# Performance work log

Hardware: AMD Instinct MI355X
Metric: run time of the kernel (lower is better)

The kernel has to match this reference:

```python
import jax, jax.numpy as jnp
import numpy as np

B, T, D = 16, 2048, 512
DB, K, TOPK, WIN = 128, 7, 16, 64
GATE_CAP = 0.5
STRAND_CAP = 0.5
_PHI = 1.618033988749895
_PSI = -0.6180339887498949


def _ln(x, w, b):
    mu = jnp.mean(x, -1, keepdims=True)
    var = jnp.var(x, -1, keepdims=True)
    return (x - mu) * jax.lax.rsqrt(var + 1e-5) * w + b


def setup_inputs() -> dict:
    key = jax.random.key(0)
    ks = jax.random.split(key, 20)
    def nrm(i, shape, scale=1.0):
        return jax.random.normal(ks[i], shape, dtype=jnp.float32) * jnp.float32(scale)
    return {
        'X_write': nrm(0, (B, T, D)),
        'X_read': nrm(1, (B, T, D)),
        'slots': nrm(2, (B, K, DB)),
        'W0': nrm(3, (D, D), D ** -0.5),
        'ln_write_w': jnp.ones((D,), jnp.float32),
        'ln_write_b': jnp.zeros((D,), jnp.float32),
        'W_V': nrm(4, (D, DB), D ** -0.5),
        'W_K_slot': nrm(5, (DB, DB), DB ** -0.5),
        'slot_key_bias': nrm(6, (K, DB), 2.0),
        'W_gate_w': nrm(7, (2 * DB, DB), (2 * DB) ** -0.5),
        'W_gate_b': jnp.full((DB,), -2.0, jnp.float32),
        'ln_strand_w': jnp.ones((DB,), jnp.float32),
        'ln_strand_b': jnp.zeros((DB,), jnp.float32),
        'Ws_Q': nrm(8, (DB, DB), DB ** -0.5),
        'Ws_K': nrm(9, (DB, DB), DB ** -0.5),
        'Ws_V': nrm(10, (DB, DB), DB ** -0.5),
        'lambda_strand': nrm(11, (DB,), 0.5),
        'W_Q_read': nrm(12, (D, DB), D ** -0.5),
        'W_K_read': nrm(13, (DB, DB), DB ** -0.5),
        'W_V_read': nrm(14, (DB, D), DB ** -0.5),
        'render_coeffs': nrm(15, (K, 3, D), 0.2),
        'slot_temps': jnp.ones((K,), jnp.float32),
    }


def _forward(X_write, X_read, slots, W0, ln_write_w, ln_write_b, W_V, W_K_slot,
             slot_key_bias, W_gate_w, W_gate_b, ln_strand_w, ln_strand_b,
             Ws_Q, Ws_K, Ws_V, lambda_strand, W_Q_read, W_K_read, W_V_read,
             render_coeffs, slot_temps):
    scale = jnp.float32(DB ** -0.5)
    W0_sg = jax.lax.stop_gradient(W0)
    X_n = _ln(X_write, ln_write_w, ln_write_b)

    # ---- windowed salience + topk pair selection (no-grad in original) ----
    X_nsg = jax.lax.stop_gradient(X_n)
    X_W0 = X_nsg @ W0_sg.T                      # [B,T,D]
    NEG = jnp.float32(-1e30)
    sal = []
    for o in range(1, WIN + 1):                 # offset j = i - o, fixed small loop
        s = jnp.sum(X_nsg[:, o:, :] * X_W0[:, :-o, :], axis=-1)  # [B, T-o]
        sal.append(jnp.pad(s, ((0, 0), (o, 0)), constant_values=NEG))
    sal = jnp.stack(sal, axis=-1).reshape(B, T * WIN)
    _, flat_idx = jax.lax.top_k(sal, TOPK)      # [B, TOPK]
    i_idx = flat_idx // WIN
    j_idx = i_idx - (flat_idx % WIN + 1)

    # ---- gather pairs, salience-weighted relation vector ----
    x_newer = jnp.take_along_axis(X_n, i_idx[:, :, None], axis=1)   # [B,TOPK,D]
    x_older = jnp.take_along_axis(X_n, j_idx[:, :, None], axis=1)
    pair_sal = jnp.sum(x_newer * (x_older @ W0_sg.T), axis=-1)      # [B,TOPK]
    alpha = jax.nn.softmax(pair_sal, axis=-1)
    rel = (x_newer - x_older) @ W_V                                 # [B,TOPK,DB]
    R_t = jnp.einsum('bk,bkd->bd', alpha, rel)                      # [B,DB]

    # ---- gated slot write ----
    slot_keys = slots @ W_K_slot + slot_key_bias                    # [B,K,DB]
    compat = jnp.einsum('bkd,bd->bk', slot_keys, R_t) * scale * jax.nn.softplus(slot_temps)
    sw = jax.nn.softmax(compat, axis=-1)
    weighted_R = sw[:, :, None] * R_t[:, None, :]                   # [B,K,DB]
    g = jax.nn.sigmoid(jnp.concatenate([slots, weighted_R], -1) @ W_gate_w + W_gate_b)
    slots_upd = (1.0 - g) * slots + g * weighted_R

    # ---- K x K strand mixer ----
    Bn = _ln(slots_upd, ln_strand_w, ln_strand_b)
    sa = jax.nn.softmax(jnp.einsum('bqd,bkd->bqk', Bn @ Ws_Q, Bn @ Ws_K) * scale, axis=-1)
    ctx = sa @ (Bn @ Ws_V)
    slots_next = slots_upd + ctx * jnp.clip(jnp.tanh(lambda_strand), -STRAND_CAP, STRAND_CAP)

    # ---- aux losses ----
    L_persist = jnp.mean((slots_next - slots) ** 2)
    nrm = jnp.maximum(jnp.linalg.norm(slots_next, axis=-1, keepdims=True), 1e-12)
    Bnorm = slots_next / nrm
    cos = jnp.einsum('bkd,bjd->bkj', Bnorm, Bnorm)
    off = ~jnp.eye(K, dtype=bool)
    L_div = jnp.mean((cos ** 2)[:, off])

    # ---- directional gated read attention ----
    q_r = X_read @ W_Q_read                                         # [B,T,DB]
    k_r = slots_next @ W_K_read                                     # [B,K,DB]
    v_r = slots_next @ W_V_read                                     # [B,K,D]
    scores = jnp.einsum('btd,bkd->btk', q_r, k_r) * scale
    q_mean = jnp.mean(X_read, axis=1)                               # [B,D]
    w0q = q_mean @ W0_sg.T
    denom = jnp.float32(_PHI - _PSI)
    phi_q = (w0q - _PSI * q_mean) / denom
    psi_q = (_PHI * q_mean - w0q) / denom
    phi_mag = jnp.linalg.norm(phi_q, axis=-1, keepdims=True)
    psi_mag = jnp.linalg.norm(psi_q, axis=-1, keepdims=True)
    total = phi_mag + psi_mag + 1e-6
    basis = jnp.concatenate([jnp.ones_like(phi_mag), phi_mag / total, psi_mag / total], -1)  # [B,3]
    gate = jnp.clip(jnp.tanh(jnp.einsum('bi,kid->bkd', basis, render_coeffs)), -GATE_CAP, GATE_CAP)
    z = jnp.einsum('btk,bkd->btd', jax.nn.softmax(scores, axis=-1), v_r * gate)
    return z, slots_next, L_persist, L_div


def reference(X_write, X_read, slots, W0, ln_write_w, ln_write_b, W_V, W_K_slot,
              slot_key_bias, W_gate_w, W_gate_b, ln_strand_w, ln_strand_b,
              Ws_Q, Ws_K, Ws_V, lambda_strand, W_Q_read, W_K_read, W_V_read,
              render_coeffs, slot_temps):
    return _forward(X_write, X_read, slots, W0, ln_write_w, ln_write_b, W_V, W_K_slot,
                    slot_key_bias, W_gate_w, W_gate_b, ln_strand_w, ln_strand_b,
                    Ws_Q, Ws_K, Ws_V, lambda_strand, W_Q_read, W_K_read, W_V_read,
                    render_coeffs, slot_temps)
```

## Files before the change

kernel.cpp:

```cpp
#include <hip/hip_runtime.h>
#include <math.h>

#define B_ 16
#define T_ 2048
#define D_ 512
#define DB_ 128
#define K_ 7
#define TOPK_ 16
#define WIN_ 64

static constexpr float SCALE_ = 0.08838834764831845f;
static constexpr float PHI_ = 1.618033988749895f;
static constexpr float PSI_ = -0.6180339887498949f;
static constexpr float INV_DENOM_ = 0.4472135954999579f;
static constexpr float NEGV = -1e30f;
static constexpr float NEGINF = -3.402823466e38f;

typedef __attribute__((ext_vector_type(8))) __bf16 bf16x8;
typedef __attribute__((ext_vector_type(8))) unsigned short u16x8;
typedef __attribute__((ext_vector_type(4))) float f32x4;

__device__ inline float softplusf(float x){
    return fmaxf(x, 0.f) + log1pf(expf(-fabsf(x)));
}
__device__ inline unsigned short f2bf(float x){
    unsigned int u = __float_as_uint(x);
    unsigned int r = (u + 0x7FFFu + ((u >> 16) & 1u)) >> 16;
    return (unsigned short)r;
}
__device__ inline float bf2f(unsigned short h){
    return __uint_as_float(((unsigned int)h) << 16);
}
__device__ inline bf16x8 ld_bf8(const unsigned short* p){
    u16x8 r = *(const u16x8*)p;
    return __builtin_bit_cast(bf16x8, r);
}
__device__ inline unsigned int pkbf(float a, float b){
    unsigned int r;
    asm("v_cvt_pk_bf16_f32 %0, %1, %2" : "=v"(r) : "v"(a), "v"(b));
    return r;
}
typedef __attribute__((address_space(3))) unsigned int as3_u32;
typedef const __attribute__((address_space(1))) unsigned int as1_u32c;
__device__ inline void gload16(const void* g, void* l){
    __builtin_amdgcn_global_load_lds((as1_u32c*)g, (as3_u32*)l, 16, 0, 0);
}

__global__ __launch_bounds__(256) void prep_kernel(const float* __restrict__ X,
                                                   const float* __restrict__ w,
                                                   const float* __restrict__ b,
                                                   unsigned short* __restrict__ Xh,
                                                   unsigned short* __restrict__ Xl,
                                                   const float* __restrict__ W0,
                                                   unsigned short* __restrict__ Wh,
                                                   unsigned short* __restrict__ Wl,
                                                   const float* __restrict__ Xr,
                                                   float* __restrict__ qpart)
{
    int bx = blockIdx.x;
    int tid = threadIdx.x;
    if (bx < 4096) {
        int lane = tid & 63, wv = tid >> 6;
        int row = bx * 8 + wv * 2;
        float4 wv0 = *(const float4*)(w + lane*4);
        float4 wv1 = *(const float4*)(w + 256 + lane*4);
        float4 bv0 = *(const float4*)(b + lane*4);
        float4 bv1 = *(const float4*)(b + 256 + lane*4);
        #pragma unroll
        for (int rr = 0; rr < 2; rr++) {
            const float* x = X + (size_t)(row + rr) * D_;
            float4 v0 = *(const float4*)(x + lane*4);
            float4 v1 = *(const float4*)(x + 256 + lane*4);
            float s  = v0.x+v0.y+v0.z+v0.w + v1.x+v1.y+v1.z+v1.w;
            float ss = v0.x*v0.x+v0.y*v0.y+v0.z*v0.z+v0.w*v0.w
                     + v1.x*v1.x+v1.y*v1.y+v1.z*v1.z+v1.w*v1.w;
            #pragma unroll
            for (int off = 32; off; off >>= 1) { s += __shfl_xor(s, off); ss += __shfl_xor(ss, off); }
            float mu = s * (1.f/512.f);
            float rs = rsqrtf(ss*(1.f/512.f) - mu*mu + 1e-5f);
            float o0 = (v0.x - mu)*rs*wv0.x + bv0.x;
            float o1 = (v0.y - mu)*rs*wv0.y + bv0.y;
            float o2 = (v0.z - mu)*rs*wv0.z + bv0.z;
            float o3 = (v0.w - mu)*rs*wv0.w + bv0.w;
            float o4 = (v1.x - mu)*rs*wv1.x + bv1.x;
            float o5 = (v1.y - mu)*rs*wv1.y + bv1.y;
            float o6 = (v1.z - mu)*rs*wv1.z + bv1.z;
            float o7 = (v1.w - mu)*rs*wv1.w + bv1.w;
            unsigned short h0 = f2bf(o0), h1 = f2bf(o1), h2 = f2bf(o2), h3 = f2bf(o3);
            unsigned short h4 = f2bf(o4), h5 = f2bf(o5), h6 = f2bf(o6), h7 = f2bf(o7);
            uint2 hA; hA.x = (unsigned int)h0 | ((unsigned int)h1 << 16);
                      hA.y = (unsigned int)h2 | ((unsigned int)h3 << 16);
            uint2 hB; hB.x = (unsigned int)h4 | ((unsigned int)h5 << 16);
                      hB.y = (unsigned int)h6 | ((unsigned int)h7 << 16);
            uint2 lA; lA.x = (unsigned int)f2bf(o0 - bf2f(h0)) | ((unsigned int)f2bf(o1 - bf2f(h1)) << 16);
                      lA.y = (unsigned int)f2bf(o2 - bf2f(h2)) | ((unsigned int)f2bf(o3 - bf2f(h3)) << 16);
            uint2 lB; lB.x = (unsigned int)f2bf(o4 - bf2f(h4)) | ((unsigned int)f2bf(o5 - bf2f(h5)) << 16);
                      lB.y = (unsigned int)f2bf(o6 - bf2f(h6)) | ((unsigned int)f2bf(o7 - bf2f(h7)) << 16);
            unsigned short* xh = Xh + (size_t)(row + rr) * D_;
            unsigned short* xl = Xl + (size_t)(row + rr) * D_;
            *(uint2*)(xh + lane*4) = hA;
            *(uint2*)(xh + 256 + lane*4) = hB;
            *(uint2*)(xl + lane*4) = lA;
            *(uint2*)(xl + 256 + lane*4) = lB;
        }
    } else if (bx < 4352) {
        int gid = (bx - 4096) * 256 + tid;
        float4 v = ((const float4*)W0)[gid];
        unsigned short h0 = f2bf(v.x), h1 = f2bf(v.y), h2 = f2bf(v.z), h3 = f2bf(v.w);
        ushort4 hv = make_ushort4(h0, h1, h2, h3);
        ushort4 lv = make_ushort4(f2bf(v.x - bf2f(h0)), f2bf(v.y - bf2f(h1)),
                                  f2bf(v.z - bf2f(h2)), f2bf(v.w - bf2f(h3)));
        *(ushort4*)&Wh[(size_t)gid*4] = hv;
        *(ushort4*)&Wl[(size_t)gid*4] = lv;
    } else {
        int idx = bx - 4352;
        int b_ = idx >> 5, c = idx & 31;
        const float* base = Xr + ((size_t)(b_*T_ + c*64)) * D_;
        float s0 = 0.f, s1 = 0.f;
        for (int t = 0; t < 64; t++) {
            s0 += base[(size_t)t*D_ + tid];
            s1 += base[(size_t)t*D_ + tid + 256];
        }
        qpart[((size_t)b_*32 + c)*D_ + tid] = s0;
        qpart[((size_t)b_*32 + c)*D_ + tid + 256] = s1;
    }
}

__global__ __launch_bounds__(256) void gemm_xw0_mfma(const unsigned short* __restrict__ Ah,
                                                     const unsigned short* __restrict__ Al,
                                                     const unsigned short* __restrict__ Wh,
                                                     const unsigned short* __restrict__ Wl,
                                                     float* __restrict__ Cf)
{
    __shared__ __align__(16) unsigned short sAh[128*32], sAl[128*32], sBh[128*32], sBl[128*32];
    int t0 = blockIdx.x * 128, d0 = blockIdx.y * 128;
    int tid = threadIdx.x;
    int lane = tid & 63, wid = tid >> 6;
    int wr = wid >> 1, wc = wid & 1;
    int fr = lane & 15;
    int kc2 = ((((lane >> 4) + (fr >> 1)) & 3) * 8);

    f32x4 acc[4][4];
    #pragma unroll
    for (int m = 0; m < 4; m++)
        #pragma unroll
        for (int n = 0; n < 4; n++) acc[m][n] = (f32x4){0.f,0.f,0.f,0.f};

    const unsigned short* gs = (wid==0) ? Ah : (wid==1) ? Al : (wid==2) ? Wh : Wl;
    unsigned short* ls = (wid==0) ? sAh : (wid==1) ? sAl : (wid==2) ? sBh : sBl;
    int rowoff = (wid < 2) ? t0 : d0;
    int cch = ((lane & 3) - ((lane >> 3) & 3)) & 3;
    const unsigned short* gbase = gs + (size_t)(rowoff + (lane >> 2))*512 + cch*8;

    for (int kk = 0; kk < 512; kk += 32) {
        #pragma unroll
        for (int i = 0; i < 8; i++)
            gload16(gbase + (size_t)(16*i)*512 + kk, ls + i*512);
        __syncthreads();

        bf16x8 ahf[4], alf[4], bhf[4], blf[4];
        #pragma unroll
        for (int m = 0; m < 4; m++) {
            int r = (wr*64 + m*16 + fr)*32 + kc2;
            ahf[m] = ld_bf8(&sAh[r]);
            alf[m] = ld_bf8(&sAl[r]);
        }
        #pragma unroll
        for (int n = 0; n < 4; n++) {
            int r = (wc*64 + n*16 + fr)*32 + kc2;
            bhf[n] = ld_bf8(&sBh[r]);
            blf[n] = ld_bf8(&sBl[r]);
        }
        #pragma unroll
        for (int m = 0; m < 4; m++)
            #pragma unroll
            for (int n = 0; n < 4; n++) {
                acc[m][n] = __builtin_amdgcn_mfma_f32_16x16x32_bf16(bhf[n], ahf[m], acc[m][n], 0, 0, 0);
                acc[m][n] = __builtin_amdgcn_mfma_f32_16x16x32_bf16(bhf[n], alf[m], acc[m][n], 0, 0, 0);
                acc[m][n] = __builtin_amdgcn_mfma_f32_16x16x32_bf16(blf[n], ahf[m], acc[m][n], 0, 0, 0);
            }
        __syncthreads();
    }

    #pragma unroll
    for (int m = 0; m < 4; m++) {
        int t = t0 + wr*64 + m*16 + fr;
        #pragma unroll
        for (int n = 0; n < 4; n++) {
            int dbase = d0 + wc*64 + n*16 + (lane >> 4)*4;
            *(f32x4*)&Cf[(size_t)t*512 + dbase] = acc[m][n];
        }
    }
}

__global__ __launch_bounds__(256) void sal_mfma(const unsigned short* __restrict__ Xh,
                                                const unsigned short* __restrict__ Xl,
                                                const float* __restrict__ Cf,
                                                float* __restrict__ sal)
{
    int b = blockIdx.x, i0 = blockIdx.y * 64;
    __shared__ __align__(16) unsigned short sAh[64*32], sAl[64*32], sBh[128*32], sBl[128*32];
    int tid = threadIdx.x;
    int lane = tid & 63, wcw = tid >> 6;
    int fr = lane & 15;
    int kc2 = ((((lane >> 4) + (fr >> 1)) & 3) * 8);

    const unsigned short* XhB = Xh + (size_t)b*T_*D_;
    const unsigned short* XlB = Xl + (size_t)b*T_*D_;
    const float* CfB = Cf + (size_t)b*T_*D_;

    f32x4 acc[4][2];
    #pragma unroll
    for (int m = 0; m < 4; m++) { acc[m][0] = (f32x4){0.f,0.f,0.f,0.f}; acc[m][1] = (f32x4){0.f,0.f,0.f,0.f}; }

    int ar = tid >> 2, ac = tid & 3;
    int aslot = (ac + (ar >> 1)) & 3;
    int brow = tid >> 1, bhh = tid & 1;
    int jrow = i0 - 64 + brow;

    for (int kk = 0; kk < 512; kk += 32) {
        *(uint4*)&sAh[ar*32 + aslot*8] = *(const uint4*)(XhB + (size_t)(i0 + ar)*512 + kk + ac*8);
        *(uint4*)&sAl[ar*32 + aslot*8] = *(const uint4*)(XlB + (size_t)(i0 + ar)*512 + kk + ac*8);
        #pragma unroll
        for (int cc = 0; cc < 2; cc++) {
            int c = 2*bhh + cc;
            int slot = (c + (brow >> 1)) & 3;
            uint4 hv, lv;
            if (jrow >= 0) {
                const float* src = CfB + (size_t)jrow*512 + kk + c*8;
                float4 v0 = *(const float4*)src;
                float4 v1 = *(const float4*)(src + 4);
                unsigned int h01 = pkbf(v0.x, v0.y), h23 = pkbf(v0.z, v0.w);
                unsigned int h45 = pkbf(v1.x, v1.y), h67 = pkbf(v1.z, v1.w);
                float r0 = v0.x - __uint_as_float(h01 << 16);
                float r1 = v0.y - __uint_as_float(h01 & 0xFFFF0000u);
                float r2 = v0.z - __uint_as_float(h23 << 16);
                float r3 = v0.w - __uint_as_float(h23 & 0xFFFF0000u);
                float r4 = v1.x - __uint_as_float(h45 << 16);
                float r5 = v1.y - __uint_as_float(h45 & 0xFFFF0000u);
                float r6 = v1.z - __uint_as_float(h67 << 16);
                float r7 = v1.w - __uint_as_float(h67 & 0xFFFF0000u);
                hv.x = h01; hv.y = h23; hv.z = h45; hv.w = h67;
                lv.x = pkbf(r0, r1); lv.y = pkbf(r2, r3); lv.z = pkbf(r4, r5); lv.w = pkbf(r6, r7);
            } else {
                hv = make_uint4(0,0,0,0); lv = make_uint4(0,0,0,0);
            }
            *(uint4*)&sBh[brow*32 + slot*8] = hv;
            *(uint4*)&sBl[brow*32 + slot*8] = lv;
        }
        __syncthreads();

        bf16x8 ahf[4], alf[4], bhf[2], blf[2];
        #pragma unroll
        for (int m = 0; m < 4; m++) {
            int r = (m*16 + fr)*32 + kc2;
            ahf[m] = ld_bf8(&sAh[r]);
            alf[m] = ld_bf8(&sAl[r]);
        }
        #pragma unroll
        for (int n = 0; n < 2; n++) {
            int r = (wcw*32 + n*16 + fr)*32 + kc2;
            bhf[n] = ld_bf8(&sBh[r]);
            blf[n] = ld_bf8(&sBl[r]);
        }
        #pragma unroll
        for (int m = 0; m < 4; m++)
            #pragma unroll
            for (int n = 0; n < 2; n++) {
                acc[m][n] = __builtin_amdgcn_mfma_f32_16x16x32_bf16(ahf[m], bhf[n], acc[m][n], 0, 0, 0);
                acc[m][n] = __builtin_amdgcn_mfma_f32_16x16x32_bf16(ahf[m], blf[n], acc[m][n], 0, 0, 0);
                acc[m][n] = __builtin_amdgcn_mfma_f32_16x16x32_bf16(alf[m], bhf[n], acc[m][n], 0, 0, 0);
            }
        __syncthreads();
    }

    float* salB = sal + (size_t)b*T_*WIN_;
    #pragma unroll
    for (int m = 0; m < 4; m++) {
        #pragma unroll
        for (int n = 0; n < 2; n++) {
            int jl = wcw*32 + n*16 + fr;
            #pragma unroll
            for (int r = 0; r < 4; r++) {
                int il = m*16 + (lane >> 4)*4 + r;
                int o = il - jl + 64;
                if (o >= 1 && o <= 64) {
                    int jg = i0 - 64 + jl;
                    salB[(size_t)(i0 + il)*WIN_ + (o - 1)] = (jg >= 0) ? acc[m][n][r] : NEGV;
                }
            }
        }
    }
}

__global__ __launch_bounds__(256) void topk_stage1(const float* __restrict__ sal,
                                                   float* __restrict__ cv, int* __restrict__ ci)
{
    int b = blockIdx.x, c = blockIdx.y;
    const float* s = sal + (size_t)b*(T_*WIN_) + (size_t)c*2048;
    int base = c*2048;
    int tid = threadIdx.x;
    int lane = tid & 63, wvi = tid >> 6;
    float lv[8]; int li[8];
    #pragma unroll
    for (int k = 0; k < 8; k++) { lv[k] = NEGINF; li[k] = 0x7FFFFFFF; }
    #pragma unroll
    for (int r = 0; r < 8; r++) {
        int p = tid + r*256;
        float v = s[p];
        int idx = base + p;
        if (v > lv[7]) {
            int k = 7;
            while (k > 0 && lv[k-1] < v) { lv[k] = lv[k-1]; li[k] = li[k-1]; k--; }
            lv[k] = v; li[k] = idx;
        }
    }
    float* cvo = cv + (((size_t)b*64 + c)*64) + wvi*16;
    int*   cio = ci + (((size_t)b*64 + c)*64) + wvi*16;
    int head = 0;
    for (int r = 0; r < 16; r++) {
        float bv = (head < 8) ? lv[head] : NEGINF;
        int   bi = (head < 8) ? li[head] : 0x7FFFFFFF;
        float wv_ = bv; int wi = bi;
        #pragma unroll
        for (int off = 1; off < 64; off <<= 1) {
            float v2 = __shfl_xor(wv_, off);
            int   i2 = __shfl_xor(wi, off);
            if (v2 > wv_ || (v2 == wv_ && i2 < wi)) { wv_ = v2; wi = i2; }
        }
        if (bv == wv_ && bi == wi) head++;
        if (lane == 0) { cvo[r] = wv_; cio[r] = wi; }
    }
}

__global__ __launch_bounds__(1024) void slot_kernel(
    const unsigned short* __restrict__ Xh, const unsigned short* __restrict__ Xl,
    const float* __restrict__ slots_in,
    const float* __restrict__ cv, const int* __restrict__ ci,
    const float* __restrict__ W_V, const float* __restrict__ W_K_slot, const float* __restrict__ skb,
    const float* __restrict__ Wg, const float* __restrict__ Wgb,
    const float* __restrict__ lnw, const float* __restrict__ lnb,
    const float* __restrict__ WsQ, const float* __restrict__ WsK, const float* __restrict__ WsV,
    const float* __restrict__ lambda_, const float* __restrict__ temps,
    float* __restrict__ snws, float* __restrict__ out_slots,
    float* __restrict__ lpP, float* __restrict__ lpD)
{
    int b = blockIdx.x, tid = threadIdx.x;
    int lane = tid & 63, wvi = tid >> 6;
    __shared__ float alpha[16];
    __shared__ int   tis[16], tjs[16];
    __shared__ float tvv[16]; __shared__ int tii[16];
    __shared__ float scv[256]; __shared__ int sci[256];
    __shared__ float y[D_];
    __shared__ float part[8][DB_];
    __shared__ float pf[1024];
    __shared__ float Rt[DB_];
    __shared__ float sl[K_][DB_];
    __shared__ float upd[K_][DB_];
    __shared__ float Bn[K_][DB_];
    __shared__ float qq[K_][DB_], kk2[K_][DB_], vv[K_][DB_];
    __shared__ float snsh[K_][DB_];
    __shared__ float swv[K_], compat[K_], mu7[K_], rs7[K_], nr7[K_], ldv[K_];
    __shared__ float sa[K_][K_];

    for (int p = tid; p < K_*DB_; p += 1024) sl[p>>7][p&127] = slots_in[(size_t)b*K_*DB_ + p];

    {
        const float* cvb = cv + (size_t)b*4096;
        const int*   cib = ci + (size_t)b*4096;
        float lv[4]; int li[4];
        #pragma unroll
        for (int k = 0; k < 4; k++) { lv[k] = NEGINF; li[k] = 0x7FFFFFFF; }
        #pragma unroll
        for (int r = 0; r < 4; r++) {
            int p = tid + r*1024;
            float v = cvb[p];
            int idx = cib[p];
            if (v > lv[3] || (v == lv[3] && idx < li[3])) {
                int k = 3;
                while (k > 0 && (lv[k-1] < v || (lv[k-1] == v && li[k-1] > idx))) {
                    lv[k] = lv[k-1]; li[k] = li[k-1]; k--;
                }
                lv[k] = v; li[k] = idx;
            }
        }
        int head = 0;
        for (int r = 0; r < 16; r++) {
            float bv = (head < 4) ? lv[head] : NEGINF;
            int   bi = (head < 4) ? li[head] : 0x7FFFFFFF;
            float wv_ = bv; int wi = bi;
            #pragma unroll
            for (int off = 1; off < 64; off <<= 1) {
                float v2 = __shfl_xor(wv_, off);
                int   i2 = __shfl_xor(wi, off);
                if (v2 > wv_ || (v2 == wv_ && i2 < wi)) { wv_ = v2; wi = i2; }
            }
            if (bv == wv_ && bi == wi) head++;
            if (lane == 0) { scv[wvi*16 + r] = wv_; sci[wvi*16 + r] = wi; }
        }
        __syncthreads();
        if (wvi == 0) {
            float mv[4]; int mi[4];
            #pragma unroll
            for (int k = 0; k < 4; k++) { mv[k] = NEGINF; mi[k] = 0x7FFFFFFF; }
            #pragma unroll
            for (int r = 0; r < 4; r++) {
                int p = lane + r*64;
                float v = scv[p]; int idx = sci[p];
                if (v > mv[3] || (v == mv[3] && idx < mi[3])) {
                    int k = 3;
                    while (k > 0 && (mv[k-1] < v || (mv[k-1] == v && mi[k-1] > idx))) {
                        mv[k] = mv[k-1]; mi[k] = mi[k-1]; k--;
                    }
                    mv[k] = v; mi[k] = idx;
                }
            }
            int head2 = 0;
            for (int r = 0; r < 16; r++) {
                float bv = (head2 < 4) ? mv[head2] : NEGINF;
                int   bi = (head2 < 4) ? mi[head2] : 0x7FFFFFFF;
                float wv_ = bv; int wi = bi;
                #pragma unroll
                for (int off = 1; off < 64; off <<= 1) {
                    float v2 = __shfl_xor(wv_, off);
                    int   i2 = __shfl_xor(wi, off);
                    if (v2 > wv_ || (v2 == wv_ && i2 < wi)) { wv_ = v2; wi = i2; }
                }
                if (bv == wv_ && bi == wi) head2++;
                if (lane == 0) { tvv[r] = wv_; tii[r] = wi; }
            }
        }
        __syncthreads();
    }
    if (tid < 16) {
        float v = tvv[tid];
        int flat = tii[tid];
        tis[tid] = flat >> 6;
        tjs[tid] = (flat >> 6) - ((flat & 63) + 1);
        float m = v;
        #pragma unroll
        for (int off = 8; off; off >>= 1) m = fmaxf(m, __shfl_xor(m, off, 16));
        float e = expf(v - m);
        float s = e;
        #pragma unroll
        for (int off = 8; off; off >>= 1) s += __shfl_xor(s, off, 16);
        alpha[tid] = e / s;
    }
    __syncthreads();

    if (tid < D_) {
        float acc = 0.f;
        #pragma unroll
        for (int k = 0; k < 16; k++) {
            int i = tis[k], j = tjs[k];
            float xi = bf2f(Xh[((size_t)b*T_ + i)*D_ + tid]) + bf2f(Xl[((size_t)b*T_ + i)*D_ + tid]);
            float xj = bf2f(Xh[((size_t)b*T_ + j)*D_ + tid]) + bf2f(Xl[((size_t)b*T_ + j)*D_ + tid]);
            acc += alpha[k] * (xi - xj);
        }
        y[tid] = acc;
    }
    __syncthreads();

    {
        int g = tid >> 7, d = tid & 127;
        float acc = 0.f;
        int e0 = g * 64;
        for (int e = e0; e < e0 + 64; e++) acc += y[e] * W_V[(size_t)e*DB_ + d];
        part[g][d] = acc;
    }
    __syncthreads();
    if (tid < DB_) {
        float acc = 0.f;
        #pragma unroll
        for (int g = 0; g < 8; g++) acc += part[g][tid];
        Rt[tid] = acc;
    }
    __syncthreads();

    if (tid < K_*DB_) {
        int k = tid >> 7, d = tid & 127;
        float acc = skb[k*DB_ + d];
        for (int e = 0; e < DB_; e++) acc += sl[k][e] * W_K_slot[(size_t)e*DB_ + d];
        qq[k][d] = acc * Rt[d];
    }
    __syncthreads();
    if (wvi < K_) {
        float acc = qq[wvi][lane] + qq[wvi][lane + 64];
        #pragma unroll
        for (int off = 32; off; off >>= 1) acc += __shfl_xor(acc, off);
        if (lane == 0) compat[wvi] = acc * SCALE_ * softplusf(temps[wvi]);
    }
    __syncthreads();
    if (tid == 0) {
        float m = compat[0];
        for (int k = 1; k < K_; k++) m = fmaxf(m, compat[k]);
        float ssum = 0.f;
        for (int k = 0; k < K_; k++) { float e = expf(compat[k]-m); swv[k] = e; ssum += e; }
        for (int k = 0; k < K_; k++) swv[k] /= ssum;
    }
    __syncthreads();

    if (tid < K_*DB_) {
        int k = tid >> 7, d = tid & 127;
        float swk = swv[k];
        float acc = Wgb[d];
        for (int e = 0; e < DB_; e++) acc += sl[k][e] * Wg[(size_t)e*DB_ + d];
        for (int e = 0; e < DB_; e++) acc += swk * Rt[e] * Wg[(size_t)(DB_+e)*DB_ + d];
        float g = 1.f / (1.f + expf(-acc));
        upd[k][d] = (1.f - g) * sl[k][d] + g * (swk * Rt[d]);
    }
    __syncthreads();

    if (wvi < K_) {
        float v0 = upd[wvi][lane], v1 = upd[wvi][lane + 64];
        float s = v0 + v1, ss = v0*v0 + v1*v1;
        #pragma unroll
        for (int off = 32; off; off >>= 1) { s += __shfl_xor(s, off); ss += __shfl_xor(ss, off); }
        if (lane == 0) {
            float mu = s / (float)DB_;
            mu7[wvi] = mu;
            rs7[wvi] = rsqrtf(ss/(float)DB_ - mu*mu + 1e-5f);
        }
    }
    __syncthreads();
    if (tid < K_*DB_) {
        int k = tid >> 7, d = tid & 127;
        Bn[k][d] = (upd[k][d] - mu7[k]) * rs7[k] * lnw[d] + lnb[d];
    }
    __syncthreads();

    if (tid < K_*DB_) {
        int k = tid >> 7, d = tid & 127;
        float aq = 0.f, ak = 0.f, av = 0.f;
        for (int e = 0; e < DB_; e++) {
            float bn = Bn[k][e];
            aq += bn * WsQ[(size_t)e*DB_ + d];
            ak += bn * WsK[(size_t)e*DB_ + d];
            av += bn * WsV[(size_t)e*DB_ + d];
        }
        qq[k][d] = aq; kk2[k][d] = ak; vv[k][d] = av;
    }
    __syncthreads();

    if (wvi < K_) {
        int j = lane >> 3, s = lane & 7;
        float acc = 0.f;
        if (j < K_) {
            int e0 = s * 16;
            for (int e = e0; e < e0 + 16; e++) acc += qq[wvi][e] * kk2[j][e];
        }
        #pragma unroll
        for (int off = 4; off; off >>= 1) acc += __shfl_xor(acc, off, 8);
        if (s == 0 && j < K_) sa[wvi][j] = acc * SCALE_;
    }
    __syncthreads();
    if (tid < K_) {
        float m = sa[tid][0];
        for (int j = 1; j < K_; j++) m = fmaxf(m, sa[tid][j]);
        float ssum = 0.f;
        for (int j = 0; j < K_; j++) { float e = expf(sa[tid][j]-m); sa[tid][j] = e; ssum += e; }
        for (int j = 0; j < K_; j++) sa[tid][j] /= ssum;
    }
    __syncthreads();

    if (tid < K_*DB_) {
        int k = tid >> 7, d = tid & 127;
        float lam = tanhf(lambda_[d]);
        lam = fminf(fmaxf(lam, -0.5f), 0.5f);
        float c = 0.f;
        #pragma unroll
        for (int j = 0; j < K_; j++) c += sa[k][j] * vv[j][d];
        float sn = upd[k][d] + c * lam;
        snsh[k][d] = sn;
        snws[((size_t)b*K_ + k)*DB_ + d] = sn;
        out_slots[((size_t)b*K_ + k)*DB_ + d] = sn;
    }
    __syncthreads();

    {
        float dsq = 0.f;
        if (tid < K_*DB_) {
            int k = tid >> 7, d = tid & 127;
            float dd = snsh[k][d] - sl[k][d];
            dsq = dd*dd;
        }
        pf[tid] = dsq;
        if (wvi < K_) {
            float v0 = snsh[wvi][lane], v1 = snsh[wvi][lane + 64];
            float ss = v0*v0 + v1*v1;
            #pragma unroll
            for (int off = 32; off; off >>= 1) ss += __shfl_xor(ss, off);
            if (lane == 0) nr7[wvi] = fmaxf(sqrtf(ss), 1e-12f);
        }
        __syncthreads();
        if (wvi == 0) {
            float s = 0.f;
            #pragma unroll
            for (int q = 0; q < 16; q++) s += pf[lane + q*64];
            #pragma unroll
            for (int off = 32; off; off >>= 1) s += __shfl_xor(s, off);
            if (lane == 0) lpP[b] = s;
        }
        if (wvi >= 1 && wvi <= K_) {
            int q = wvi - 1;
            float accq = 0.f;
            for (int j = 0; j < K_; j++) {
                if (j == q) continue;
                float dt = snsh[q][lane]*snsh[j][lane] + snsh[q][lane+64]*snsh[j][lane+64];
                #pragma unroll
                for (int off = 32; off; off >>= 1) dt += __shfl_xor(dt, off);
                float cs = dt / (nr7[q] * nr7[j]);
                accq += cs*cs;
            }
            if (lane == 0) ldv[q] = accq;
        }
        __syncthreads();
        if (tid == 0) {
            float s = 0.f;
            for (int q = 0; q < K_; q++) s += ldv[q];
            lpD[b] = s;
        }
    }
}

__global__ __launch_bounds__(256) void w0q_part_kernel(const float* __restrict__ qpart,
                                                       const float* __restrict__ W0,
                                                       float* __restrict__ w0p)
{
    int b = blockIdx.x, c = blockIdx.y, tid = threadIdx.x;
    __shared__ float qm[D_];
    for (int p = tid; p < D_; p += 256) {
        float s = 0.f;
        for (int cc = 0; cc < 32; cc++) s += qpart[((size_t)b*32 + cc)*D_ + p];
        qm[p] = s * (1.f/2048.f);
    }
    __syncthreads();
    int w = tid >> 6, lane = tid & 63;
    float ph = 0.f, ps = 0.f;
    for (int r = 0; r < 16; r++) {
        int d = c*64 + w*16 + r;
        const float* wr = W0 + (size_t)d*D_;
        float s = 0.f;
        #pragma unroll
        for (int q = 0; q < 8; q++) s += qm[lane + q*64] * wr[lane + q*64];
        #pragma unroll
        for (int off = 32; off; off >>= 1) s += __shfl_xor(s, off);
        float phi = (s - PSI_*qm[d]) * INV_DENOM_;
        float psi = (PHI_*qm[d] - s) * INV_DENOM_;
        ph += phi*phi; ps += psi*psi;
    }
    __shared__ float shp[4], shs[4];
    if (lane == 0) { shp[w] = ph; shs[w] = ps; }
    __syncthreads();
    if (tid == 0) {
        w0p[((size_t)b*8 + c)*2 + 0] = shp[0]+shp[1]+shp[2]+shp[3];
        w0p[((size_t)b*8 + c)*2 + 1] = shs[0]+shs[1]+shs[2]+shs[3];
    }
}

__global__ __launch_bounds__(256) void kqvg_kernel(
    const float* __restrict__ sn, const float* __restrict__ WKr,
    const float* __restrict__ WQr, const float* __restrict__ WVr,
    const float* __restrict__ rc, const float* __restrict__ w0p,
    const float* __restrict__ lpP, const float* __restrict__ lpD,
    float* __restrict__ kq, float* __restrict__ vg, float* __restrict__ loss_out)
{
    int b = blockIdx.x, k = blockIdx.y, tid = threadIdx.x;
    if (b == 0 && k == 0 && tid == 0) {
        float s = 0.f, s2 = 0.f;
        for (int bb = 0; bb < B_; bb++) { s += lpP[bb]; s2 += lpD[bb]; }
        loss_out[0] = s / (float)(B_*K_*DB_);
        loss_out[1] = s2 / (float)(B_*(K_*K_-K_));
    }
    float P = 0.f, Q = 0.f;
    #pragma unroll
    for (int c = 0; c < 8; c++) {
        P += w0p[((size_t)b*8 + c)*2 + 0];
        Q += w0p[((size_t)b*8 + c)*2 + 1];
    }
    float pm = sqrtf(P), qm2 = sqrtf(Q);
    float tot = pm + qm2 + 1e-6f;
    float b1 = pm / tot, b2 = qm2 / tot;

    __shared__ float sl[DB_], kr[DB_];
    if (tid < DB_) sl[tid] = sn[((size_t)b*K_ + k)*DB_ + tid];
    __syncthreads();
    if (tid < DB_) {
        float a = 0.f;
        for (int e = 0; e < DB_; e++) a += sl[e] * WKr[(size_t)e*DB_ + tid];
        kr[tid] = a;
    }
    __syncthreads();
    #pragma unroll
    for (int rep = 0; rep < 2; rep++) {
        int e = tid + rep*256;
        float a = 0.f;
        const float* wq = WQr + (size_t)e*DB_;
        for (int d = 0; d < DB_; d++) a += kr[d] * wq[d];
        kq[((size_t)b*K_ + k)*D_ + e] = a;
    }
    #pragma unroll
    for (int rep = 0; rep < 2; rep++) {
        int dd = tid + rep*256;
        float a = 0.f;
        for (int e = 0; e < DB_; e++) a += sl[e] * WVr[(size_t)e*D_ + dd];
        float gpre = rc[((size_t)k*3 + 0)*D_ + dd] + b1*rc[((size_t)k*3 + 1)*D_ + dd] + b2*rc[((size_t)k*3 + 2)*D_ + dd];
        float g = tanhf(gpre);
        g = fminf(fmaxf(g, -0.5f), 0.5f);
        vg[((size_t)b*K_ + k)*D_ + dd] = a * g;
    }
}

__global__ __launch_bounds__(256) void z_kernel(const float* __restrict__ Xr,
                                                const float* __restrict__ kq,
                                                const float* __restrict__ vg,
                                                float* __restrict__ z)
{
    int b = blockIdx.x;
    int t0 = blockIdx.y * 64;
    __shared__ float kqs[K_][D_];
    __shared__ float vgs[K_][D_];
    int tid = threadIdx.x;
    for (int p = tid; p < K_*D_; p += 256) {
        kqs[p>>9][p&511] = kq[(size_t)b*K_*D_ + p];
        vgs[p>>9][p&511] = vg[(size_t)b*K_*D_ + p];
    }
    __syncthreads();
    int lane = tid & 63, w = tid >> 6;
    for (int it = 0; it < 16; it++) {
        int t = t0 + w*16 + it;
        const float* x = Xr + ((size_t)b*T_ + t)*D_;
        float xr[8];
        float s[K_] = {0,0,0,0,0,0,0};
        #pragma unroll
        for (int r = 0; r < 8; r++) {
            int e = lane + r*64;
            xr[r] = x[e];
            #pragma unroll
            for (int k = 0; k < K_; k++) s[k] += xr[r] * kqs[k][e];
        }
        #pragma unroll
        for (int k = 0; k < K_; k++)
            for (int off = 32; off; off >>= 1) s[k] += __shfl_xor(s[k], off);
        float sc[K_];
        float m = NEGINF;
        #pragma unroll
        for (int k = 0; k < K_; k++) { sc[k] = s[k] * SCALE_; m = fmaxf(m, sc[k]); }
        float p[K_], ssum = 0.f;
        #pragma unroll
        for (int k = 0; k < K_; k++) { p[k] = expf(sc[k] - m); ssum += p[k]; }
        float inv = 1.f / ssum;
        float* zp = z + ((size_t)b*T_ + t)*D_;
        #pragma unroll
        for (int r = 0; r < 8; r++) {
            int e = lane + r*64;
            float a = 0.f;
            #pragma unroll
            for (int k = 0; k < K_; k++) a += p[k] * vgs[k][e];
            zp[e] = a * inv;
        }
    }
}

extern "C" void kernel_launch(void* const* d_in, const int* in_sizes, int n_in,
                              void* d_out, int out_size, void* d_ws, size_t ws_size,
                              hipStream_t stream)
{
    const float* X_write = (const float*)d_in[0];
    const float* X_read  = (const float*)d_in[1];
    const float* slots   = (const float*)d_in[2];
    const float* W0      = (const float*)d_in[3];
    const float* lnw_w   = (const float*)d_in[4];
    const float* lnw_b   = (const float*)d_in[5];
    const float* W_V     = (const float*)d_in[6];
    const float* W_K_slot= (const float*)d_in[7];
    const float* skb     = (const float*)d_in[8];
    const float* Wg      = (const float*)d_in[9];
    const float* Wgb     = (const float*)d_in[10];
    const float* lns_w   = (const float*)d_in[11];
    const float* lns_b   = (const float*)d_in[12];
    const float* WsQ     = (const float*)d_in[13];
    const float* WsK     = (const float*)d_in[14];
    const float* WsV     = (const float*)d_in[15];
    const float* lambda_ = (const float*)d_in[16];
    const float* WQr     = (const float*)d_in[17];
    const float* WKr     = (const float*)d_in[18];
    const float* WVr     = (const float*)d_in[19];
    const float* rc      = (const float*)d_in[20];
    const float* temps   = (const float*)d_in[21];

    const size_t NXD = (size_t)B_*T_*D_;
    unsigned short* Xh  = (unsigned short*)d_ws;
    unsigned short* Xl  = Xh + NXD;
    float* Cf           = (float*)(Xl + NXD);
    unsigned short* W0h = (unsigned short*)(Cf + NXD);
    unsigned short* W0l = W0h + (size_t)D_*D_;
    float* fscr  = (float*)(W0l + (size_t)D_*D_);
    float* qpart = fscr;
    float* w0p   = qpart + (size_t)B_*32*D_;
    float* snws  = w0p + 256;
    float* kq    = snws + (size_t)B_*K_*DB_;
    float* vg    = kq + (size_t)B_*K_*D_;
    float* cv    = vg + (size_t)B_*K_*D_;
    int*   ci    = (int*)(cv + (size_t)B_*64*64);
    float* lpP   = (float*)(ci + (size_t)B_*64*64);
    float* lpD   = lpP + 16;

    float* z_out     = (float*)d_out;
    float* slots_out = z_out + NXD;
    float* loss_out  = slots_out + (size_t)B_*K_*DB_;
    float* sal       = z_out;

    prep_kernel<<<dim3(4096 + 256 + 512), dim3(256), 0, stream>>>(
        X_write, lnw_w, lnw_b, Xh, Xl, W0, W0h, W0l, X_read, qpart);
    gemm_xw0_mfma<<<dim3(B_*T_/128, D_/128), dim3(256), 0, stream>>>(Xh, Xl, W0h, W0l, Cf);
    sal_mfma<<<dim3(B_, T_/64), dim3(256), 0, stream>>>(Xh, Xl, Cf, sal);
    topk_stage1<<<dim3(B_, 64), dim3(256), 0, stream>>>(sal, cv, ci);
    slot_kernel<<<dim3(B_), dim3(1024), 0, stream>>>(Xh, Xl, slots, cv, ci,
        W_V, W_K_slot, skb, Wg, Wgb, lns_w, lns_b, WsQ, WsK, WsV, lambda_, temps,
        snws, slots_out, lpP, lpD);
    w0q_part_kernel<<<dim3(B_, 8), dim3(256), 0, stream>>>(qpart, W0, w0p);
    kqvg_kernel<<<dim3(B_, K_), dim3(256), 0, stream>>>(snws, WKr, WQr, WVr, rc, w0p,
        lpP, lpD, kq, vg, loss_out);
    z_kernel<<<dim3(B_, T_/64), dim3(256), 0, stream>>>(X_read, kq, vg, z_out);
}
```

Measured before the change: 288.1 us.

## Double-buffer GEMM and salience loads, fold w0q into topk launch

The X·W0 GEMM now double-buffers its shared-memory tiles, so the next K-slice is fetched while the current one feeds MFMA, and one barrier per iteration is dropped. The salience kernel prefetches the next slice's global data into registers before running the current slice's MFMAs, and converts to bf16 hi/lo when writing to shared memory. The w0q_part work moves into extra blocks of topk_stage1, removing one kernel launch. The trade-off is doubled LDS use in the GEMM, which may lower occupancy, and higher register pressure in sal_mfma.

```diff
diff --git a/kernel.cpp b/kernel.cpp
--- a/kernel.cpp
+++ b/kernel.cpp
@@ -132,7 +132,7 @@
                                                      const unsigned short* __restrict__ Wl,
                                                      float* __restrict__ Cf)
 {
-    __shared__ __align__(16) unsigned short sAh[128*32], sAl[128*32], sBh[128*32], sBl[128*32];
+    __shared__ __align__(16) unsigned short sAh[2*128*32], sAl[2*128*32], sBh[2*128*32], sBl[2*128*32];
     int t0 = blockIdx.x * 128, d0 = blockIdx.y * 128;
     int tid = threadIdx.x;
     int lane = tid & 63, wid = tid >> 6;
@@ -147,27 +147,36 @@
         for (int n = 0; n < 4; n++) acc[m][n] = (f32x4){0.f,0.f,0.f,0.f};
 
     const unsigned short* gs = (wid==0) ? Ah : (wid==1) ? Al : (wid==2) ? Wh : Wl;
-    unsigned short* ls = (wid==0) ? sAh : (wid==1) ? sAl : (wid==2) ? sBh : sBl;
+    unsigned short* lsA = (wid==0) ? sAh : (wid==1) ? sAl : (wid==2) ? sBh : sBl;
     int rowoff = (wid < 2) ? t0 : d0;
     int cch = ((lane & 3) - ((lane >> 3) & 3)) & 3;
     const unsigned short* gbase = gs + (size_t)(rowoff + (lane >> 2))*512 + cch*8;
 
-    for (int kk = 0; kk < 512; kk += 32) {
-        #pragma unroll
-        for (int i = 0; i < 8; i++)
-            gload16(gbase + (size_t)(16*i)*512 + kk, ls + i*512);
+    #pragma unroll
+    for (int i = 0; i < 8; i++)
+        gload16(gbase + (size_t)(16*i)*512 + 0, lsA + i*512);
+
+    for (int t = 0; t < 16; t++) {
+        int cur = t & 1;
         __syncthreads();
-
+        if (t < 15) {
+            unsigned short* ls = lsA + (cur^1)*(128*32);
+            int kk = (t+1)*32;
+            #pragma unroll
+            for (int i = 0; i < 8; i++)
+                gload16(gbase + (size_t)(16*i)*512 + kk, ls + i*512);
+        }
+        int bo = cur*(128*32);
         bf16x8 ahf[4], alf[4], bhf[4], blf[4];
         #pragma unroll
         for (int m = 0; m < 4; m++) {
-            int r = (wr*64 + m*16 + fr)*32 + kc2;
+            int r = bo + (wr*64 + m*16 + fr)*32 + kc2;
             ahf[m] = ld_bf8(&sAh[r]);
             alf[m] = ld_bf8(&sAl[r]);
         }
         #pragma unroll
         for (int n = 0; n < 4; n++) {
-            int r = (wc*64 + n*16 + fr)*32 + kc2;
+            int r = bo + (wc*64 + n*16 + fr)*32 + kc2;
             bhf[n] = ld_bf8(&sBh[r]);
             blf[n] = ld_bf8(&sBl[r]);
         }
@@ -179,7 +188,6 @@
                 acc[m][n] = __builtin_amdgcn_mfma_f32_16x16x32_bf16(bhf[n], alf[m], acc[m][n], 0, 0, 0);
                 acc[m][n] = __builtin_amdgcn_mfma_f32_16x16x32_bf16(blf[n], ahf[m], acc[m][n], 0, 0, 0);
             }
-        __syncthreads();
     }
 
     #pragma unroll
@@ -218,38 +226,56 @@
     int brow = tid >> 1, bhh = tid & 1;
     int jrow = i0 - 64 + brow;
 
-    for (int kk = 0; kk < 512; kk += 32) {
-        *(uint4*)&sAh[ar*32 + aslot*8] = *(const uint4*)(XhB + (size_t)(i0 + ar)*512 + kk + ac*8);
-        *(uint4*)&sAl[ar*32 + aslot*8] = *(const uint4*)(XlB + (size_t)(i0 + ar)*512 + kk + ac*8);
+    uint4 rAh, rAl;
+    float4 rB0[2], rB1[2];
+
+    auto LOAD = [&](int kk){
+        rAh = *(const uint4*)(XhB + (size_t)(i0 + ar)*512 + kk + ac*8);
+        rAl = *(const uint4*)(XlB + (size_t)(i0 + ar)*512 + kk + ac*8);
+        #pragma unroll
+        for (int cc = 0; cc < 2; cc++) {
+            int c = 2*bhh + cc;
+            if (jrow >= 0) {
+                const float* src = CfB + (size_t)jrow*512 + kk + c*8;
+                rB0[cc] = *(const float4*)src;
+                rB1[cc] = *(const float4*)(src + 4);
+            } else {
+                rB0[cc] = make_float4(0.f,0.f,0.f,0.f);
+                rB1[cc] = make_float4(0.f,0.f,0.f,0.f);
+            }
+        }
+    };
+    auto WRITE = [&](){
+        *(uint4*)&sAh[ar*32 + aslot*8] = rAh;
+        *(uint4*)&sAl[ar*32 + aslot*8] = rAl;
         #pragma unroll
         for (int cc = 0; cc < 2; cc++) {
             int c = 2*bhh + cc;
             int slot = (c + (brow >> 1)) & 3;
             uint4 hv, lv;
-            if (jrow >= 0) {
-                const float* src = CfB + (size_t)jrow*512 + kk + c*8;
-                float4 v0 = *(const float4*)src;
-                float4 v1 = *(const float4*)(src + 4);
-                unsigned int h01 = pkbf(v0.x, v0.y), h23 = pkbf(v0.z, v0.w);
-                unsigned int h45 = pkbf(v1.x, v1.y), h67 = pkbf(v1.z, v1.w);
-                float r0 = v0.x - __uint_as_float(h01 << 16);
-                float r1 = v0.y - __uint_as_float(h01 & 0xFFFF0000u);
-                float r2 = v0.z - __uint_as_float(h23 << 16);
-                float r3 = v0.w - __uint_as_float(h23 & 0xFFFF0000u);
-                float r4 = v1.x - __uint_as_float(h45 << 16);
-                float r5 = v1.y - __uint_as_float(h45 & 0xFFFF0000u);
-                float r6 = v1.z - __uint_as_float(h67 << 16);
-                float r7 = v1.w - __uint_as_float(h67 & 0xFFFF0000u);
-                hv.x = h01; hv.y = h23; hv.z = h45; hv.w = h67;
-                lv.x = pkbf(r0, r1); lv.y = pkbf(r2, r3); lv.z = pkbf(r4, r5); lv.w = pkbf(r6, r7);
-            } else {
-                hv = make_uint4(0,0,0,0); lv = make_uint4(0,0,0,0);
-            }
+            float4 v0 = rB0[cc], v1 = rB1[cc];
+            unsigned int h01 = pkbf(v0.x, v0.y), h23 = pkbf(v0.z, v0.w);
+            unsigned int h45 = pkbf(v1.x, v1.y), h67 = pkbf(v1.z, v1.w);
+            float r0 = v0.x - __uint_as_float(h01 << 16);
+            float r1 = v0.y - __uint_as_float(h01 & 0xFFFF0000u);
+            float r2 = v0.z - __uint_as_float(h23 << 16);
+            float r3 = v0.w - __uint_as_float(h23 & 0xFFFF0000u);
+            float r4 = v1.x - __uint_as_float(h45 << 16);
+            float r5 = v1.y - __uint_as_float(h45 & 0xFFFF0000u);
+            float r6 = v1.z - __uint_as_float(h67 << 16);
+            float r7 = v1.w - __uint_as_float(h67 & 0xFFFF0000u);
+            hv.x = h01; hv.y = h23; hv.z = h45; hv.w = h67;
+            lv.x = pkbf(r0, r1); lv.y = pkbf(r2, r3); lv.z = pkbf(r4, r5); lv.w = pkbf(r6, r7);
             *(uint4*)&sBh[brow*32 + slot*8] = hv;
             *(uint4*)&sBl[brow*32 + slot*8] = lv;
         }
+    };
+
+    LOAD(0);
+    for (int t = 0; t < 16; t++) {
+        WRITE();
         __syncthreads();
-
+        int kkn = (t+1)*32;
         bf16x8 ahf[4], alf[4], bhf[2], blf[2];
         #pragma unroll
         for (int m = 0; m < 4; m++) {
@@ -263,6 +289,7 @@
             bhf[n] = ld_bf8(&sBh[r]);
             blf[n] = ld_bf8(&sBl[r]);
         }
+        if (t < 15) LOAD(kkn);
         #pragma unroll
         for (int m = 0; m < 4; m++)
             #pragma unroll
@@ -294,12 +321,47 @@
 }
 
 __global__ __launch_bounds__(256) void topk_stage1(const float* __restrict__ sal,
-                                                   float* __restrict__ cv, int* __restrict__ ci)
+                                                   float* __restrict__ cv, int* __restrict__ ci,
+                                                   const float* __restrict__ qpart,
+                                                   const float* __restrict__ W0,
+                                                   float* __restrict__ w0p)
 {
-    int b = blockIdx.x, c = blockIdx.y;
+    int b = blockIdx.x, tid = threadIdx.x;
+    if (blockIdx.y >= 64) {
+        int c = blockIdx.y - 64;
+        __shared__ float qm[D_];
+        for (int p = tid; p < D_; p += 256) {
+            float s = 0.f;
+            for (int cc = 0; cc < 32; cc++) s += qpart[((size_t)b*32 + cc)*D_ + p];
+            qm[p] = s * (1.f/2048.f);
+        }
+        __syncthreads();
+        int w = tid >> 6, lane = tid & 63;
+        float ph = 0.f, ps = 0.f;
+        for (int r = 0; r < 16; r++) {
+            int d = c*64 + w*16 + r;
+            const float* wr = W0 + (size_t)d*D_;
+            float s = 0.f;
+            #pragma unroll
+            for (int q = 0; q < 8; q++) s += qm[lane + q*64] * wr[lane + q*64];
+            #pragma unroll
+            for (int off = 32; off; off >>= 1) s += __shfl_xor(s, off);
+            float phi = (s - PSI_*qm[d]) * INV_DENOM_;
+            float psi = (PHI_*qm[d] - s) * INV_DENOM_;
+            ph += phi*phi; ps += psi*psi;
+        }
+        __shared__ float shp[4], shs[4];
+        if (lane == 0) { shp[w] = ph; shs[w] = ps; }
+        __syncthreads();
+        if (tid == 0) {
+            w0p[((size_t)b*8 + c)*2 + 0] = shp[0]+shp[1]+shp[2]+shp[3];
+            w0p[((size_t)b*8 + c)*2 + 1] = shs[0]+shs[1]+shs[2]+shs[3];
+        }
+        return;
+    }
+    int c = blockIdx.y;
     const float* s = sal + (size_t)b*(T_*WIN_) + (size_t)c*2048;
     int base = c*2048;
-    int tid = threadIdx.x;
     int lane = tid & 63, wvi = tid >> 6;
     float lv[8]; int li[8];
     #pragma unroll
@@ -623,41 +685,6 @@
     }
 }
 
-__global__ __launch_bounds__(256) void w0q_part_kernel(const float* __restrict__ qpart,
-                                                       const float* __restrict__ W0,
-                                                       float* __restrict__ w0p)
-{
-    int b = blockIdx.x, c = blockIdx.y, tid = threadIdx.x;
-    __shared__ float qm[D_];
-    for (int p = tid; p < D_; p += 256) {
-        float s = 0.f;
-        for (int cc = 0; cc < 32; cc++) s += qpart[((size_t)b*32 + cc)*D_ + p];
-        qm[p] = s * (1.f/2048.f);
-    }
-    __syncthreads();
-    int w = tid >> 6, lane = tid & 63;
-    float ph = 0.f, ps = 0.f;
-    for (int r = 0; r < 16; r++) {
-        int d = c*64 + w*16 + r;
-        const float* wr = W0 + (size_t)d*D_;
-        float s = 0.f;
-        #pragma unroll
-        for (int q = 0; q < 8; q++) s += qm[lane + q*64] * wr[lane + q*64];
-        #pragma unroll
-        for (int off = 32; off; off >>= 1) s += __shfl_xor(s, off);
-        float phi = (s - PSI_*qm[d]) * INV_DENOM_;
-        float psi = (PHI_*qm[d] - s) * INV_DENOM_;
-        ph += phi*phi; ps += psi*psi;
-    }
-    __shared__ float shp[4], shs[4];
-    if (lane == 0) { shp[w] = ph; shs[w] = ps; }
-    __syncthreads();
-    if (tid == 0) {
-        w0p[((size_t)b*8 + c)*2 + 0] = shp[0]+shp[1]+shp[2]+shp[3];
-        w0p[((size_t)b*8 + c)*2 + 1] = shs[0]+shs[1]+shs[2]+shs[3];
-    }
-}
-
 __global__ __launch_bounds__(256) void kqvg_kernel(
     const float* __restrict__ sn, const float* __restrict__ WKr,
     const float* __restrict__ WQr, const float* __restrict__ WVr,
@@ -815,11 +842,10 @@
         X_write, lnw_w, lnw_b, Xh, Xl, W0, W0h, W0l, X_read, qpart);
     gemm_xw0_mfma<<<dim3(B_*T_/128, D_/128), dim3(256), 0, stream>>>(Xh, Xl, W0h, W0l, Cf);
     sal_mfma<<<dim3(B_, T_/64), dim3(256), 0, stream>>>(Xh, Xl, Cf, sal);
-    topk_stage1<<<dim3(B_, 64), dim3(256), 0, stream>>>(sal, cv, ci);
+    topk_stage1<<<dim3(B_, 72), dim3(256), 0, stream>>>(sal, cv, ci, qpart, W0, w0p);
     slot_kernel<<<dim3(B_), dim3(1024), 0, stream>>>(Xh, Xl, slots, cv, ci,
         W_V, W_K_slot, skb, Wg, Wgb, lns_w, lns_b, WsQ, WsK, WsV, lambda_, temps,
         snws, slots_out, lpP, lpD);
-    w0q_part_kernel<<<dim3(B_, 8), dim3(256), 0, stream>>>(qpart, W0, w0p);
     kqvg_kernel<<<dim3(B_, K_), dim3(256), 0, stream>>>(snws, WKr, WQr, WVr, rc, w0p,
         lpP, lpD, kq, vg, loss_out);
     z_kernel<<<dim3(B_, T_/64), dim3(256), 0, stream>>>(X_read, kq, vg, z_out);
```

New measurement: 269.9 us. 6.3% less time.
